# Kernel tuning notes

Hardware: AMD Instinct MI355X
Metric: run time of the kernel (lower is better)

The kernel has to match this reference:

```python
import jax, jax.numpy as jnp
import numpy as np
from jax.ops import segment_sum, segment_max

DIM = 32   # hidden dim (hardcoded in Net)
N = 10000  # nodes
E = 160000 # edges
B = 64     # graphs in batch


def setup_inputs():
    key = jax.random.key(0)
    ks = jax.random.split(key, 16)
    r = lambda k, s: jax.random.normal(k, s, dtype=jnp.float32) * 0.1
    z = lambda s: jnp.zeros(s, jnp.float32)
    return {
        "x": jax.random.normal(ks[0], (N, 1), jnp.float32),
        "edge_attr": jax.random.normal(ks[1], (E, 2), jnp.float32),
        "lin0_w": r(ks[2], (1, DIM)), "lin0_b": z((DIM,)),
        "nn_w1": r(ks[3], (2, 128)), "nn_b1": z((128,)),
        "nn_w2": r(ks[4], (128, DIM * DIM)), "nn_b2": z((DIM * DIM,)),
        "conv_root": r(ks[5], (DIM, DIM)), "conv_bias": z((DIM,)),
        "gru_w_ih": r(ks[6], (DIM, 3 * DIM)), "gru_w_hh": r(ks[7], (DIM, 3 * DIM)),
        "gru_b_ih": z((3 * DIM,)), "gru_b_hh": z((3 * DIM,)),
        "lstm_w_ih": r(ks[8], (2 * DIM, 4 * DIM)), "lstm_w_hh": r(ks[9], (DIM, 4 * DIM)),
        "lstm_b_ih": z((4 * DIM,)), "lstm_b_hh": z((4 * DIM,)),
        "lin1_w": r(ks[10], (2 * DIM, DIM)), "lin1_b": z((DIM,)),
        "lin2_w": r(ks[11], (DIM, 1)), "lin2_b": z((1,)),
        "edge_index": jax.random.randint(ks[12], (2, E), 0, N),
        "batch": jnp.sort(jax.random.randint(ks[13], (N,), 0, B)),
    }


def _forward(x, edge_attr, params, edge_index, batch):
    (lin0_w, lin0_b, nn_w1, nn_b1, nn_w2, nn_b2, conv_root, conv_bias,
     gru_w_ih, gru_w_hh, gru_b_ih, gru_b_hh,
     lstm_w_ih, lstm_w_hh, lstm_b_ih, lstm_b_hh,
     lin1_w, lin1_b, lin2_w, lin2_b) = params
    src, dst = edge_index[0], edge_index[1]
    deg = jnp.maximum(segment_sum(jnp.ones((E,), x.dtype), dst, num_segments=N), 1.0)[:, None]
    # edge-conditioned weight matrices (depend only on edge_attr -> compute once)
    ew = (jax.nn.relu(edge_attr @ nn_w1 + nn_b1) @ nn_w2 + nn_b2).reshape(E, DIM, DIM)

    out = jax.nn.relu(x @ lin0_w + lin0_b)  # (N, DIM)
    h = out                                  # GRU hidden state
    for _ in range(3):
        # NNConv: gather -> per-edge matmul -> scatter-mean, plus root weight + bias
        msg = jnp.einsum('ei,eio->eo', out[src], ew)          # (E, DIM)
        agg = segment_sum(msg, dst, num_segments=N) / deg      # (N, DIM)
        m = jax.nn.relu(agg + out @ conv_root + conv_bias)
        # single GRU step (seq_len = 1)
        gi = m @ gru_w_ih + gru_b_ih
        gh = h @ gru_w_hh + gru_b_hh
        i_r, i_z, i_n = jnp.split(gi, 3, axis=-1)
        h_r, h_z, h_n = jnp.split(gh, 3, axis=-1)
        rg = jax.nn.sigmoid(i_r + h_r)
        zg = jax.nn.sigmoid(i_z + h_z)
        ng = jnp.tanh(i_n + rg * h_n)
        h = (1.0 - zg) * ng + zg * h
        out = h

    # Set2Set pooling, 3 processing steps
    q_star = jnp.zeros((B, 2 * DIM), x.dtype)
    hh = jnp.zeros((B, DIM), x.dtype)
    cc = jnp.zeros((B, DIM), x.dtype)
    for _ in range(3):
        gates = q_star @ lstm_w_ih + lstm_b_ih + hh @ lstm_w_hh + lstm_b_hh
        ig, fg, gg, og = jnp.split(gates, 4, axis=-1)  # torch gate order i,f,g,o
        cc = jax.nn.sigmoid(fg) * cc + jax.nn.sigmoid(ig) * jnp.tanh(gg)
        hh = jax.nn.sigmoid(og) * jnp.tanh(cc)
        q = hh                                          # (B, DIM)
        e = jnp.sum(out * q[batch], axis=-1)            # (N,)
        a = jnp.exp(e - segment_max(e, batch, num_segments=B)[batch])
        a = a / segment_sum(a, batch, num_segments=B)[batch]
        rvec = segment_sum(a[:, None] * out, batch, num_segments=B)  # (B, DIM)
        q_star = jnp.concatenate([q, rvec], axis=-1)

    y = jax.nn.relu(q_star @ lin1_w + lin1_b)
    return (y @ lin2_w + lin2_b).reshape(-1)  # (B,)


def reference(x, edge_attr, lin0_w, lin0_b, nn_w1, nn_b1, nn_w2, nn_b2, conv_root, conv_bias, gru_w_ih, gru_w_hh, gru_b_ih, gru_b_hh, lstm_w_ih, lstm_w_hh, lstm_b_ih, lstm_b_hh, lin1_w, lin1_b, lin2_w, lin2_b, edge_index, batch):
    params = (lin0_w, lin0_b, nn_w1, nn_b1, nn_w2, nn_b2, conv_root, conv_bias,
              gru_w_ih, gru_w_hh, gru_b_ih, gru_b_hh,
              lstm_w_ih, lstm_w_hh, lstm_b_ih, lstm_b_hh,
              lin1_w, lin1_b, lin2_w, lin2_b)
    return _forward(x, edge_attr, params, edge_index, batch)
```

## Files before the change

kernel.cpp:

```cpp
#include <hip/hip_runtime.h>
#include <math.h>

#define NN 10000
#define NE 160000
#define NG 64
#define DIM 32
#define CAP 96
#define NBIN (CAP + 1)

typedef __attribute__((ext_vector_type(8))) short bf16x8;
typedef __attribute__((ext_vector_type(4))) float f32x4;
typedef __attribute__((ext_vector_type(2))) float f32x2;

__device__ __forceinline__ float sigmoidf_(float x) { return 1.f / (1.f + expf(-x)); }

__device__ __forceinline__ unsigned short f2bf(float x) {
    unsigned u = __float_as_uint(x);
    u += 0x7FFF + ((u >> 16) & 1);
    return (unsigned short)(u >> 16);
}
__device__ __forceinline__ float bf2f(unsigned short b) {
    return __uint_as_float(((unsigned)b) << 16);
}
__device__ __forceinline__ float rlanef(float v, int i) {
    return __uint_as_float((unsigned)__builtin_amdgcn_readlane((int)__float_as_uint(v), i));
}

__global__ void k_setup(const float* __restrict__ w2, unsigned short* __restrict__ w2f,
                        const float* __restrict__ x, const float* __restrict__ lw,
                        const float* __restrict__ lb, float* __restrict__ out,
                        const int* __restrict__ batch, int* __restrict__ gstart,
                        const int* __restrict__ ei, const float* __restrict__ ea,
                        int* __restrict__ cursor,
                        int* __restrict__ srt_src, float* __restrict__ srt_ea) {
    int b = blockIdx.x, t = threadIdx.x;
    if (b < 512) {
        int tid = b * 256 + t;
        int h = tid >> 10, rem = tid & 1023, i = rem >> 5, n = rem & 31;
        float v = w2[tid];
        unsigned short hi = f2bf(v);
        unsigned short lo = f2bf(v - bf2f(hi));
        int hp = 2 * (h & 63) + (h >> 6);
        int s = hp >> 5, hm = hp & 31, q = hm >> 3, j = hm & 7;
        int tile = n >> 4, nn = n & 15, lane = q * 16 + nn;
        int c = (i * 4 + s) * 2 + tile;
        w2f[(c * 2 + 0) * 512 + lane * 8 + j] = hi;
        w2f[(c * 2 + 1) * 512 + lane * 8 + j] = lo;
    } else if (b < 1762) {
        int idx = (b - 512) * 256 + t;
        int n = idx >> 5, d = idx & 31;
        out[idx] = fmaxf(x[n] * lw[d] + lb[d], 0.f);
    } else if (b == 1762) {
        if (t <= NG) {
            int g = t, lo = 0, hi = NN;
            while (lo < hi) { int mid = (lo + hi) >> 1; if (batch[mid] < g) lo = mid + 1; else hi = mid; }
            gstart[g] = lo;
        }
    } else {
        int e = (b - 1763) * 256 + t;
        if (e < NE) {
            int d = ei[NE + e];
            int p = atomicAdd(&cursor[d], 1);
            int pos = d * CAP + p;
            srt_src[pos] = ei[e];
            srt_ea[2 * pos]     = ea[2 * e];
            srt_ea[2 * pos + 1] = ea[2 * e + 1];
        }
    }
}

__global__ __launch_bounds__(1024) void k_perm(const int* __restrict__ cursor,
                                               int* __restrict__ perm) {
    __shared__ int hist[NBIN * 16];
    __shared__ int binsum[NBIN];
    __shared__ int base[NBIN];
    int t = threadIdx.x;
    for (int i = t; i < NBIN * 16; i += 1024) hist[i] = 0;
    __syncthreads();
    int sub = t & 15;
    for (int n = t; n < NN; n += 1024) {
        int d = cursor[n]; d = d > CAP ? CAP : d;
        atomicAdd(&hist[d * 16 + sub], 1);
    }
    __syncthreads();
    if (t < NBIN) {
        int s = 0;
        #pragma unroll
        for (int k = 0; k < 16; ++k) s += hist[t * 16 + k];
        binsum[t] = s;
    }
    __syncthreads();
    if (t == 0) {
        int acc = 0;
        for (int d = CAP; d >= 0; --d) { base[d] = acc; acc += binsum[d]; }
    }
    __syncthreads();
    if (t < NBIN) {
        int acc = base[t];
        #pragma unroll
        for (int k = 0; k < 16; ++k) {
            int c = hist[t * 16 + k];
            hist[t * 16 + k] = acc;
            acc += c;
        }
    }
    __syncthreads();
    for (int n = t; n < NN; n += 1024) {
        int d = cursor[n]; d = d > CAP ? CAP : d;
        int pos = atomicAdd(&hist[d * 16 + sub], 1);
        perm[pos] = n;
    }
}

#define NS 1040
#define PS 8320
__global__ __launch_bounds__(512, 4) void k_conv_gru(
    const int* __restrict__ perm,
    const int* __restrict__ cursor, const int* __restrict__ srt_src,
    const float* __restrict__ srt_ea,
    const float* __restrict__ w1, const float* __restrict__ b1,
    const unsigned short* __restrict__ w2f, const float* __restrict__ b2,
    const float* __restrict__ out_old,
    const float* __restrict__ root, const float* __restrict__ cbias,
    const float* __restrict__ wih, const float* __restrict__ whh,
    const float* __restrict__ bih, const float* __restrict__ bhh,
    float* __restrict__ out_new)
{
    __shared__ __align__(16) unsigned short RB[2 * PS];
    __shared__ float sSg[8][DIM];
    __shared__ int sNode[8];
    int t = threadIdx.x;
    int wave = t >> 6, lane = t & 63;
    int n0 = blockIdx.x * 8;
    int n = perm[n0 + wave];
    if (lane == 0) sNode[wave] = n;

    f32x2 acc2[32];
    #pragma unroll
    for (int i = 0; i < 32; ++i) acc2[i] = (f32x2){0.f, 0.f};
    float sacc = 0.f;

    float w1a0 = w1[lane],      w1c0 = w1[128 + lane],  bb0 = b1[lane];
    float w1a1 = w1[64 + lane], w1c1 = w1[192 + lane],  bb1 = b1[64 + lane];

    int deg = cursor[n];
    int rs = n * CAP;
    const float2* eap = (const float2*)srt_ea;

    int msrc = 0; float mex = 0.f, mey = 0.f;
    if (lane < deg) {
        msrc = srt_src[rs + lane];
        float2 a = eap[rs + lane];
        mex = a.x; mey = a.y;
    }

    int dmain = deg < 64 ? deg : 64;
    int i = 0;
    for (; i + 1 < dmain; i += 2) {
        int s0 = __builtin_amdgcn_readlane(msrc, i);
        int s1 = __builtin_amdgcn_readlane(msrc, i + 1);
        float a0x = rlanef(mex, i),     a0y = rlanef(mey, i);
        float a1x = rlanef(mex, i + 1), a1y = rlanef(mey, i + 1);
        const float* o0 = out_old + s0 * DIM;
        const float* o1 = out_old + s1 * DIM;
        f32x2 r0 = { fmaxf(a0x * w1a0 + a0y * w1c0 + bb0, 0.f),
                     fmaxf(a0x * w1a1 + a0y * w1c1 + bb1, 0.f) };
        f32x2 r1 = { fmaxf(a1x * w1a0 + a1y * w1c0 + bb0, 0.f),
                     fmaxf(a1x * w1a1 + a1y * w1c1 + bb1, 0.f) };
        #pragma unroll
        for (int q = 0; q < 32; ++q)
            acc2[q] += r0 * o0[q];
        #pragma unroll
        for (int q = 0; q < 32; ++q)
            acc2[q] += r1 * o1[q];
        const float* oc = (lane < 32) ? (o0 + lane) : (o1 + lane - 32);
        sacc += *oc;
    }
    if (i < dmain) {
        int s0 = __builtin_amdgcn_readlane(msrc, i);
        float a0x = rlanef(mex, i), a0y = rlanef(mey, i);
        const float* o0 = out_old + s0 * DIM;
        f32x2 r0 = { fmaxf(a0x * w1a0 + a0y * w1c0 + bb0, 0.f),
                     fmaxf(a0x * w1a1 + a0y * w1c1 + bb1, 0.f) };
        #pragma unroll
        for (int q = 0; q < 32; ++q)
            acc2[q] += r0 * o0[q];
        if (lane < 32) sacc += o0[lane];
    }
    for (int p = rs + 64; p < rs + deg; ++p) {
        int s0 = __builtin_amdgcn_readfirstlane(srt_src[p]);
        float2 a0 = eap[p];
        const float* o0 = out_old + s0 * DIM;
        f32x2 r0 = { fmaxf(a0.x * w1a0 + a0.y * w1c0 + bb0, 0.f),
                     fmaxf(a0.x * w1a1 + a0.y * w1c1 + bb1, 0.f) };
        #pragma unroll
        for (int q = 0; q < 32; ++q)
            acc2[q] += r0 * o0[q];
        if (lane < 32) sacc += o0[lane];
    }
    sacc += __shfl_xor(sacc, 32);
    if (lane < DIM) sSg[wave][lane] = sacc;

    int quad = lane >> 4;
    int mm = lane & 7;
    unsigned aoff = (unsigned)(mm * NS + wave * 128 + quad * 8);
    f32x4 acc0 = {0.f, 0.f, 0.f, 0.f};
    f32x4 acc1 = {0.f, 0.f, 0.f, 0.f};

    unsigned short* Hw = RB + wave * NS;
    unsigned short* Lw = RB + PS + wave * NS;

    #pragma unroll
    for (int pass = 0; pass < 4; ++pass) {
        if (pass) __syncthreads();
        #pragma unroll
        for (int li = 0; li < 8; ++li) {
            f32x2 v = acc2[pass * 8 + li];
            unsigned short h0 = f2bf(v.x);
            unsigned short l0 = f2bf(v.x - bf2f(h0));
            unsigned short h1 = f2bf(v.y);
            unsigned short l1 = f2bf(v.y - bf2f(h1));
            *(unsigned*)(Hw + li * 128 + 2 * lane) = (unsigned)h0 | ((unsigned)h1 << 16);
            *(unsigned*)(Lw + li * 128 + 2 * lane) = (unsigned)l0 | ((unsigned)l1 << 16);
        }
        __syncthreads();
        int ig = pass * 8 + wave;
        #pragma unroll
        for (int s = 0; s < 4; ++s) {
            bf16x8 ah = *(const bf16x8*)(RB + aoff + s * 32);
            bf16x8 al = *(const bf16x8*)(RB + PS + aoff + s * 32);
            const unsigned short* bp = w2f + (unsigned)((ig * 4 + s) * 2048 + lane * 8);
            bf16x8 bh0 = *(const bf16x8*)(bp);
            bf16x8 bl0 = *(const bf16x8*)(bp + 512);
            bf16x8 bh1 = *(const bf16x8*)(bp + 1024);
            bf16x8 bl1 = *(const bf16x8*)(bp + 1536);
            acc0 = __builtin_amdgcn_mfma_f32_16x16x32_bf16(ah, bh0, acc0, 0, 0, 0);
            acc0 = __builtin_amdgcn_mfma_f32_16x16x32_bf16(ah, bl0, acc0, 0, 0, 0);
            acc0 = __builtin_amdgcn_mfma_f32_16x16x32_bf16(al, bh0, acc0, 0, 0, 0);
            acc1 = __builtin_amdgcn_mfma_f32_16x16x32_bf16(ah, bh1, acc1, 0, 0, 0);
            acc1 = __builtin_amdgcn_mfma_f32_16x16x32_bf16(ah, bl1, acc1, 0, 0, 0);
            acc1 = __builtin_amdgcn_mfma_f32_16x16x32_bf16(al, bh1, acc1, 0, 0, 0);
        }
    }
    __syncthreads();

    float* part = (float*)RB;
    #pragma unroll
    for (int r = 0; r < 4; ++r) {
        part[((wave * 2 + 0) * 64 + lane) * 4 + r] = acc0[r];
        part[((wave * 2 + 1) * 64 + lane) * 4 + r] = acc1[r];
    }
    __syncthreads();

    if (t < 256) {
        int nb = t >> 5, d = t & 31;
        int nn_ = sNode[nb];
        int base = t & 32;
        int tile = d >> 4, col = d & 15;
        int lidx = (nb >> 2) * 16 + col, reg = nb & 3;
        float aggv = 0.f;
        #pragma unroll
        for (int wv = 0; wv < 8; ++wv)
            aggv += part[((wv * 2 + tile) * 64 + lidx) * 4 + reg];

        float bt = 0.f;
        #pragma unroll 8
        for (int i2 = 0; i2 < DIM; ++i2) bt += sSg[nb][i2] * b2[i2 * DIM + d];
        int cdeg = cursor[nn_];
        float degf = (float)(cdeg > 0 ? cdeg : 1);
        aggv = (aggv + bt) / degf;

        float x = out_old[nn_ * DIM + d];
        float rootsum = 0.f;
        #pragma unroll 8
        for (int k = 0; k < DIM; ++k)
            rootsum += __shfl(x, base + k) * root[k * DIM + d];
        float m = fmaxf(aggv + rootsum + cbias[d], 0.f);

        float gir = bih[d], giz = bih[DIM + d], gin = bih[2 * DIM + d];
        float ghr = bhh[d], ghz = bhh[DIM + d], ghn = bhh[2 * DIM + d];
        #pragma unroll 4
        for (int k = 0; k < DIM; ++k) {
            float mk = __shfl(m, base + k);
            float hk = __shfl(x, base + k);
            gir += mk * wih[k * 96 + d];
            giz += mk * wih[k * 96 + DIM + d];
            gin += mk * wih[k * 96 + 2 * DIM + d];
            ghr += hk * whh[k * 96 + d];
            ghz += hk * whh[k * 96 + DIM + d];
            ghn += hk * whh[k * 96 + 2 * DIM + d];
        }
        float rg = sigmoidf_(gir + ghr);
        float zg = sigmoidf_(giz + ghz);
        float ng = tanhf(gin + rg * ghn);
        out_new[nn_ * DIM + d] = (1.f - zg) * ng + zg * x;
    }
}

__global__ __launch_bounds__(256) void k_set2set(
    const float* __restrict__ out, const int* __restrict__ gstart,
    const float* __restrict__ wih, const float* __restrict__ whh,
    const float* __restrict__ bih, const float* __restrict__ bhh,
    const float* __restrict__ l1w, const float* __restrict__ l1b,
    const float* __restrict__ l2w, const float* __restrict__ l2b,
    float* __restrict__ ebuf, float* __restrict__ y)
{
    __shared__ float swih[64 * 128];
    __shared__ float swhh[32 * 128];
    __shared__ float sq[2 * DIM];
    __shared__ float shh[DIM], scc[DIM];
    __shared__ float sgates[4 * DIM];
    __shared__ float sacc[8][DIM];
    __shared__ float sredA[4], sredB[4];

    int g = blockIdx.x, t = threadIdx.x;
    {
        const float4* wv = (const float4*)wih;   float4* sv = (float4*)swih;
        for (int i = t; i < 2048; i += 256) sv[i] = wv[i];
        const float4* wv2 = (const float4*)whh;  float4* sv2 = (float4*)swhh;
        for (int i = t; i < 1024; i += 256) sv2[i] = wv2[i];
    }
    if (t < 2 * DIM) sq[t] = 0.f;
    if (t < DIM) { shh[t] = 0.f; scc[t] = 0.f; }
    int ns = gstart[g], ne = gstart[g + 1];
    __syncthreads();

    for (int step = 0; step < 3; ++step) {
        if (t < 128) {
            float acc = bih[t] + bhh[t];
            #pragma unroll 8
            for (int k = 0; k < 2 * DIM; ++k) acc += sq[k] * swih[k * 128 + t];
            #pragma unroll 8
            for (int k = 0; k < DIM; ++k)     acc += shh[k] * swhh[k * 128 + t];
            sgates[t] = acc;
        }
        __syncthreads();
        if (t < DIM) {
            float ig = sigmoidf_(sgates[t]);
            float fg = sigmoidf_(sgates[DIM + t]);
            float gg = tanhf(sgates[2 * DIM + t]);
            float og = sigmoidf_(sgates[3 * DIM + t]);
            float c_new = fg * scc[t] + ig * gg;
            float h_new = og * tanhf(c_new);
            scc[t] = c_new;
            shh[t] = h_new;
            sq[t] = h_new;
        }
        __syncthreads();

        float lmax = -3.0e38f;
        for (int n = ns + t; n < ne; n += 256) {
            const float4* orow = (const float4*)(out + n * DIM);
            float e = 0.f;
            #pragma unroll
            for (int q = 0; q < 8; ++q) {
                float4 o4 = orow[q];
                e += o4.x * shh[4 * q] + o4.y * shh[4 * q + 1]
                   + o4.z * shh[4 * q + 2] + o4.w * shh[4 * q + 3];
            }
            ebuf[n] = e;
            lmax = fmaxf(lmax, e);
        }
        #pragma unroll
        for (int s = 1; s < 64; s <<= 1) lmax = fmaxf(lmax, __shfl_xor(lmax, s));
        if ((t & 63) == 0) sredA[t >> 6] = lmax;
        __syncthreads();
        float M = fmaxf(fmaxf(sredA[0], sredA[1]), fmaxf(sredA[2], sredA[3]));

        float lsum = 0.f;
        for (int n = ns + t; n < ne; n += 256) {
            float v = expf(ebuf[n] - M);
            ebuf[n] = v;
            lsum += v;
        }
        #pragma unroll
        for (int s = 1; s < 64; s <<= 1) lsum += __shfl_xor(lsum, s);
        if ((t & 63) == 0) sredB[t >> 6] = lsum;
        __syncthreads();
        float S = sredB[0] + sredB[1] + sredB[2] + sredB[3];
        float inv = (S > 0.f) ? 1.f / S : 0.f;

        int stp = t >> 5, d = t & 31;
        float racc = 0.f;
        for (int n = ns + stp; n < ne; n += 8)
            racc += ebuf[n] * out[n * DIM + d];
        sacc[stp][d] = racc;
        __syncthreads();
        if (t < DIM) {
            float r = 0.f;
            #pragma unroll
            for (int s = 0; s < 8; ++s) r += sacc[s][t];
            sq[DIM + t] = r * inv;
        }
        __syncthreads();
    }

    if (t < DIM) {
        float h = l1b[t];
        #pragma unroll 8
        for (int k = 0; k < 2 * DIM; ++k) h += sq[k] * l1w[k * DIM + t];
        float v = fmaxf(h, 0.f) * l2w[t];
        #pragma unroll
        for (int s = 1; s < 32; s <<= 1) v += __shfl_xor(v, s);
        if (t == 0) y[g] = v + l2b[0];
    }
}

extern "C" void kernel_launch(void* const* d_in, const int* in_sizes, int n_in,
                              void* d_out, int out_size, void* d_ws, size_t ws_size,
                              hipStream_t stream) {
    const float* x         = (const float*)d_in[0];
    const float* edge_attr = (const float*)d_in[1];
    const float* lin0_w    = (const float*)d_in[2];
    const float* lin0_b    = (const float*)d_in[3];
    const float* nn_w1     = (const float*)d_in[4];
    const float* nn_b1     = (const float*)d_in[5];
    const float* nn_w2     = (const float*)d_in[6];
    const float* nn_b2     = (const float*)d_in[7];
    const float* conv_root = (const float*)d_in[8];
    const float* conv_bias = (const float*)d_in[9];
    const float* gru_w_ih  = (const float*)d_in[10];
    const float* gru_w_hh  = (const float*)d_in[11];
    const float* gru_b_ih  = (const float*)d_in[12];
    const float* gru_b_hh  = (const float*)d_in[13];
    const float* lstm_w_ih = (const float*)d_in[14];
    const float* lstm_w_hh = (const float*)d_in[15];
    const float* lstm_b_ih = (const float*)d_in[16];
    const float* lstm_b_hh = (const float*)d_in[17];
    const float* lin1_w    = (const float*)d_in[18];
    const float* lin1_b    = (const float*)d_in[19];
    const float* lin2_w    = (const float*)d_in[20];
    const float* lin2_b    = (const float*)d_in[21];
    const int*   edge_index= (const int*)d_in[22];
    const int*   batch     = (const int*)d_in[23];
    float* yout = (float*)d_out;

    char* p = (char*)d_ws;
    auto alloc = [&](size_t bytes) { char* r = p; p += (bytes + 255) & ~(size_t)255; return r; };

    int*   cursor = (int*)  alloc(NN * sizeof(int));
    size_t zero_bytes = (size_t)(p - (char*)d_ws);
    int*   gstart    = (int*)  alloc((NG + 1) * sizeof(int));
    int*   srt_src   = (int*)  alloc((size_t)NN * CAP * sizeof(int));
    float* srt_ea    = (float*)alloc((size_t)NN * CAP * 2 * sizeof(float));
    float* outA      = (float*)alloc(NN * DIM * sizeof(float));
    float* outB      = (float*)alloc(NN * DIM * sizeof(float));
    int*   perm      = (int*)  alloc(NN * sizeof(int));
    unsigned short* w2f = (unsigned short*)alloc(262144 * sizeof(unsigned short));
    float* ebuf      = (float*)alloc(NN * sizeof(float));
    (void)ws_size; (void)n_in; (void)in_sizes; (void)out_size;

    hipMemsetAsync(d_ws, 0, zero_bytes, stream);

    k_setup<<<2388, 256, 0, stream>>>(nn_w2, w2f, x, lin0_w, lin0_b, outA, batch, gstart,
                                      edge_index, edge_attr, cursor, srt_src, srt_ea);
    k_perm<<<1, 1024, 0, stream>>>(cursor, perm);

    const float* cur = outA;
    float* nxt = outB;
    for (int it = 0; it < 3; ++it) {
        k_conv_gru<<<1250, 512, 0, stream>>>(perm, cursor, srt_src, srt_ea,
                                             nn_w1, nn_b1, w2f, nn_b2,
                                             cur,
                                             conv_root, conv_bias,
                                             gru_w_ih, gru_w_hh, gru_b_ih, gru_b_hh,
                                             nxt);
        const float* tmp = nxt; nxt = (float*)cur; cur = tmp;
    }
    const float* outF = cur;

    k_set2set<<<NG, 256, 0, stream>>>(outF, gstart,
                                      lstm_w_ih, lstm_w_hh, lstm_b_ih, lstm_b_hh,
                                      lin1_w, lin1_b, lin2_w, lin2_b, ebuf, yout);
}
```

Baseline: 319.0 us.

## Split each node's hidden units across two waves in conv_gru blocks

Each node's 128-wide edge-network hidden dimension is now split across two waves, so blocks grow to 1024 threads (16 waves) and each thread keeps 32 accumulators instead of 64 packed pairs. The w2f weight layout is reordered to match the new hidden-unit ownership, and each wave runs only half of the MFMA k-slices. The partial-sum reduction now covers 16 waves. The goal is lower register pressure and more waves in flight to hide gather latency. The cost is that both waves gather the same neighbour rows, duplicating loads, and larger blocks add barrier overhead.

```diff
diff --git a/kernel.cpp b/kernel.cpp
--- a/kernel.cpp
+++ b/kernel.cpp
@@ -10,7 +10,6 @@
 
 typedef __attribute__((ext_vector_type(8))) short bf16x8;
 typedef __attribute__((ext_vector_type(4))) float f32x4;
-typedef __attribute__((ext_vector_type(2))) float f32x2;
 
 __device__ __forceinline__ float sigmoidf_(float x) { return 1.f / (1.f + expf(-x)); }
 
@@ -40,8 +39,7 @@
         float v = w2[tid];
         unsigned short hi = f2bf(v);
         unsigned short lo = f2bf(v - bf2f(hi));
-        int hp = 2 * (h & 63) + (h >> 6);
-        int s = hp >> 5, hm = hp & 31, q = hm >> 3, j = hm & 7;
+        int s = h >> 5, hm = h & 31, q = hm >> 3, j = hm & 7;
         int tile = n >> 4, nn = n & 15, lane = q * 16 + nn;
         int c = (i * 4 + s) * 2 + tile;
         w2f[(c * 2 + 0) * 512 + lane * 8 + j] = hi;
@@ -114,7 +112,7 @@
 
 #define NS 1040
 #define PS 8320
-__global__ __launch_bounds__(512, 4) void k_conv_gru(
+__global__ __launch_bounds__(1024, 8) void k_conv_gru(
     const int* __restrict__ perm,
     const int* __restrict__ cursor, const int* __restrict__ srt_src,
     const float* __restrict__ srt_ea,
@@ -130,18 +128,18 @@
     __shared__ float sSg[8][DIM];
     __shared__ int sNode[8];
     int t = threadIdx.x;
-    int wave = t >> 6, lane = t & 63;
-    int n0 = blockIdx.x * 8;
-    int n = perm[n0 + wave];
-    if (lane == 0) sNode[wave] = n;
-
-    f32x2 acc2[32];
+    int w = t >> 6, lane = t & 63;
+    int nslot = w & 7, hhalf = w >> 3;
+    int n = perm[blockIdx.x * 8 + nslot];
+    if (hhalf == 0 && lane == 0) sNode[nslot] = n;
+    int hb = hhalf * 64;
+
+    float acc[32];
     #pragma unroll
-    for (int i = 0; i < 32; ++i) acc2[i] = (f32x2){0.f, 0.f};
+    for (int q = 0; q < 32; ++q) acc[q] = 0.f;
     float sacc = 0.f;
 
-    float w1a0 = w1[lane],      w1c0 = w1[128 + lane],  bb0 = b1[lane];
-    float w1a1 = w1[64 + lane], w1c1 = w1[192 + lane],  bb1 = b1[64 + lane];
+    float w1a = w1[hb + lane], w1c = w1[128 + hb + lane], bb = b1[hb + lane];
 
     int deg = cursor[n];
     int rs = n * CAP;
@@ -163,70 +161,64 @@
         float a1x = rlanef(mex, i + 1), a1y = rlanef(mey, i + 1);
         const float* o0 = out_old + s0 * DIM;
         const float* o1 = out_old + s1 * DIM;
-        f32x2 r0 = { fmaxf(a0x * w1a0 + a0y * w1c0 + bb0, 0.f),
-                     fmaxf(a0x * w1a1 + a0y * w1c1 + bb1, 0.f) };
-        f32x2 r1 = { fmaxf(a1x * w1a0 + a1y * w1c0 + bb0, 0.f),
-                     fmaxf(a1x * w1a1 + a1y * w1c1 + bb1, 0.f) };
-        #pragma unroll
-        for (int q = 0; q < 32; ++q)
-            acc2[q] += r0 * o0[q];
-        #pragma unroll
-        for (int q = 0; q < 32; ++q)
-            acc2[q] += r1 * o1[q];
-        const float* oc = (lane < 32) ? (o0 + lane) : (o1 + lane - 32);
-        sacc += *oc;
+        float r0 = fmaxf(a0x * w1a + a0y * w1c + bb, 0.f);
+        float r1 = fmaxf(a1x * w1a + a1y * w1c + bb, 0.f);
+        #pragma unroll
+        for (int q = 0; q < 32; ++q) acc[q] += r0 * o0[q];
+        #pragma unroll
+        for (int q = 0; q < 32; ++q) acc[q] += r1 * o1[q];
+        if (hhalf == 0) {
+            const float* oc = (lane < 32) ? (o0 + lane) : (o1 + lane - 32);
+            sacc += *oc;
+        }
     }
     if (i < dmain) {
         int s0 = __builtin_amdgcn_readlane(msrc, i);
         float a0x = rlanef(mex, i), a0y = rlanef(mey, i);
         const float* o0 = out_old + s0 * DIM;
-        f32x2 r0 = { fmaxf(a0x * w1a0 + a0y * w1c0 + bb0, 0.f),
-                     fmaxf(a0x * w1a1 + a0y * w1c1 + bb1, 0.f) };
-        #pragma unroll
-        for (int q = 0; q < 32; ++q)
-            acc2[q] += r0 * o0[q];
-        if (lane < 32) sacc += o0[lane];
+        float r0 = fmaxf(a0x * w1a + a0y * w1c + bb, 0.f);
+        #pragma unroll
+        for (int q = 0; q < 32; ++q) acc[q] += r0 * o0[q];
+        if (hhalf == 0 && lane < 32) sacc += o0[lane];
     }
     for (int p = rs + 64; p < rs + deg; ++p) {
         int s0 = __builtin_amdgcn_readfirstlane(srt_src[p]);
         float2 a0 = eap[p];
         const float* o0 = out_old + s0 * DIM;
-        f32x2 r0 = { fmaxf(a0.x * w1a0 + a0.y * w1c0 + bb0, 0.f),
-                     fmaxf(a0.x * w1a1 + a0.y * w1c1 + bb1, 0.f) };
-        #pragma unroll
-        for (int q = 0; q < 32; ++q)
-            acc2[q] += r0 * o0[q];
-        if (lane < 32) sacc += o0[lane];
-    }
-    sacc += __shfl_xor(sacc, 32);
-    if (lane < DIM) sSg[wave][lane] = sacc;
+        float r0 = fmaxf(a0.x * w1a + a0.y * w1c + bb, 0.f);
+        #pragma unroll
+        for (int q = 0; q < 32; ++q) acc[q] += r0 * o0[q];
+        if (hhalf == 0 && lane < 32) sacc += o0[lane];
+    }
+    if (hhalf == 0) {
+        sacc += __shfl_xor(sacc, 32);
+        if (lane < DIM) sSg[nslot][lane] = sacc;
+    }
 
     int quad = lane >> 4;
-    int mm = lane & 7;
-    unsigned aoff = (unsigned)(mm * NS + wave * 128 + quad * 8);
+    unsigned aoff = (unsigned)((lane & 7) * NS + nslot * 128 + quad * 8);
     f32x4 acc0 = {0.f, 0.f, 0.f, 0.f};
     f32x4 acc1 = {0.f, 0.f, 0.f, 0.f};
 
-    unsigned short* Hw = RB + wave * NS;
-    unsigned short* Lw = RB + PS + wave * NS;
+    unsigned short* Hw = RB + nslot * NS + hb;
+    unsigned short* Lw = RB + PS + nslot * NS + hb;
 
     #pragma unroll
     for (int pass = 0; pass < 4; ++pass) {
         if (pass) __syncthreads();
         #pragma unroll
         for (int li = 0; li < 8; ++li) {
-            f32x2 v = acc2[pass * 8 + li];
-            unsigned short h0 = f2bf(v.x);
-            unsigned short l0 = f2bf(v.x - bf2f(h0));
-            unsigned short h1 = f2bf(v.y);
-            unsigned short l1 = f2bf(v.y - bf2f(h1));
-            *(unsigned*)(Hw + li * 128 + 2 * lane) = (unsigned)h0 | ((unsigned)h1 << 16);
-            *(unsigned*)(Lw + li * 128 + 2 * lane) = (unsigned)l0 | ((unsigned)l1 << 16);
-        }
-        __syncthreads();
-        int ig = pass * 8 + wave;
-        #pragma unroll
-        for (int s = 0; s < 4; ++s) {
+            float v = acc[pass * 8 + li];
+            unsigned short h0 = f2bf(v);
+            unsigned short l0 = f2bf(v - bf2f(h0));
+            Hw[li * 128 + lane] = h0;
+            Lw[li * 128 + lane] = l0;
+        }
+        __syncthreads();
+        int ig = pass * 8 + nslot;
+        #pragma unroll
+        for (int si = 0; si < 2; ++si) {
+            int s = hhalf * 2 + si;
             bf16x8 ah = *(const bf16x8*)(RB + aoff + s * 32);
             bf16x8 al = *(const bf16x8*)(RB + PS + aoff + s * 32);
             const unsigned short* bp = w2f + (unsigned)((ig * 4 + s) * 2048 + lane * 8);
@@ -247,8 +239,8 @@
     float* part = (float*)RB;
     #pragma unroll
     for (int r = 0; r < 4; ++r) {
-        part[((wave * 2 + 0) * 64 + lane) * 4 + r] = acc0[r];
-        part[((wave * 2 + 1) * 64 + lane) * 4 + r] = acc1[r];
+        part[((w * 2 + 0) * 64 + lane) * 4 + r] = acc0[r];
+        part[((w * 2 + 1) * 64 + lane) * 4 + r] = acc1[r];
     }
     __syncthreads();
 
@@ -260,7 +252,7 @@
         int lidx = (nb >> 2) * 16 + col, reg = nb & 3;
         float aggv = 0.f;
         #pragma unroll
-        for (int wv = 0; wv < 8; ++wv)
+        for (int wv = 0; wv < 16; ++wv)
             aggv += part[((wv * 2 + tile) * 64 + lidx) * 4 + reg];
 
         float bt = 0.f;
@@ -459,12 +451,12 @@
     const float* cur = outA;
     float* nxt = outB;
     for (int it = 0; it < 3; ++it) {
-        k_conv_gru<<<1250, 512, 0, stream>>>(perm, cursor, srt_src, srt_ea,
-                                             nn_w1, nn_b1, w2f, nn_b2,
-                                             cur,
-                                             conv_root, conv_bias,
-                                             gru_w_ih, gru_w_hh, gru_b_ih, gru_b_hh,
-                                             nxt);
+        k_conv_gru<<<1250, 1024, 0, stream>>>(perm, cursor, srt_src, srt_ea,
+                                              nn_w1, nn_b1, w2f, nn_b2,
+                                              cur,
+                                              conv_root, conv_bias,
+                                              gru_w_ih, gru_w_hh, gru_b_ih, gru_b_hh,
+                                              nxt);
         const float* tmp = nxt; nxt = (float*)cur; cur = tmp;
     }
     const float* outF = cur;
```

Result: slower. 330.0 us (+3.4%).

## Process 16 nodes per block so MFMA tiles use full 16-row A fragments

Applied to the files above, without the earlier changes.

The conv-GRU kernel now launches 1024-thread blocks that each handle 16 nodes instead of 8. The bf16 hi/lo MFMA stage uses all 16 rows of the A tile instead of replicating 8 nodes, and its k-slices are split across two wave groups. This halves the w2f weight fetches per node and the wasted MFMA rows. LDS is also re-padded (LIS/ANS strides) to reduce bank conflicts. The cost is roughly double the shared memory per block and a 16-way partial reduction, and 1024-thread blocks with launch bounds of 4 may cut occupancy and raise register pressure.

```diff
diff --git a/kernel.cpp b/kernel.cpp
--- a/kernel.cpp
+++ b/kernel.cpp
@@ -112,9 +112,10 @@
     }
 }
 
-#define NS 1040
-#define PS 8320
-__global__ __launch_bounds__(512, 4) void k_conv_gru(
+#define LIS 136
+#define ANS 1096
+#define PS2 (16 * ANS)
+__global__ __launch_bounds__(1024, 4) void k_conv_gru(
     const int* __restrict__ perm,
     const int* __restrict__ cursor, const int* __restrict__ srt_src,
     const float* __restrict__ srt_ea,
@@ -126,14 +127,13 @@
     const float* __restrict__ bih, const float* __restrict__ bhh,
     float* __restrict__ out_new)
 {
-    __shared__ __align__(16) unsigned short RB[2 * PS];
-    __shared__ float sSg[8][DIM];
-    __shared__ int sNode[8];
+    __shared__ __align__(16) unsigned short RB[2 * PS2];
+    __shared__ float sSg[16][DIM];
+    __shared__ int sNode[16];
     int t = threadIdx.x;
-    int wave = t >> 6, lane = t & 63;
-    int n0 = blockIdx.x * 8;
-    int n = perm[n0 + wave];
-    if (lane == 0) sNode[wave] = n;
+    int w = t >> 6, lane = t & 63;
+    int n = perm[blockIdx.x * 16 + w];
+    if (lane == 0) sNode[w] = n;
 
     f32x2 acc2[32];
     #pragma unroll
@@ -199,16 +199,15 @@
         if (lane < 32) sacc += o0[lane];
     }
     sacc += __shfl_xor(sacc, 32);
-    if (lane < DIM) sSg[wave][lane] = sacc;
+    if (lane < DIM) sSg[w][lane] = sacc;
 
     int quad = lane >> 4;
-    int mm = lane & 7;
-    unsigned aoff = (unsigned)(mm * NS + wave * 128 + quad * 8);
+    unsigned aoff = (unsigned)((lane & 15) * ANS + (w & 7) * LIS + quad * 8);
     f32x4 acc0 = {0.f, 0.f, 0.f, 0.f};
     f32x4 acc1 = {0.f, 0.f, 0.f, 0.f};
 
-    unsigned short* Hw = RB + wave * NS;
-    unsigned short* Lw = RB + PS + wave * NS;
+    unsigned short* Hw = RB + (unsigned)(w * ANS);
+    unsigned short* Lw = Hw + PS2;
 
     #pragma unroll
     for (int pass = 0; pass < 4; ++pass) {
@@ -220,15 +219,17 @@
             unsigned short l0 = f2bf(v.x - bf2f(h0));
             unsigned short h1 = f2bf(v.y);
             unsigned short l1 = f2bf(v.y - bf2f(h1));
-            *(unsigned*)(Hw + li * 128 + 2 * lane) = (unsigned)h0 | ((unsigned)h1 << 16);
-            *(unsigned*)(Lw + li * 128 + 2 * lane) = (unsigned)l0 | ((unsigned)l1 << 16);
-        }
-        __syncthreads();
-        int ig = pass * 8 + wave;
-        #pragma unroll
-        for (int s = 0; s < 4; ++s) {
+            *(unsigned*)(Hw + li * LIS + 2 * lane) = (unsigned)h0 | ((unsigned)h1 << 16);
+            *(unsigned*)(Lw + li * LIS + 2 * lane) = (unsigned)l0 | ((unsigned)l1 << 16);
+        }
+        __syncthreads();
+        int ig = pass * 8 + (w & 7);
+        int sb = (w >> 3) * 2;
+        #pragma unroll
+        for (int si = 0; si < 2; ++si) {
+            int s = sb + si;
             bf16x8 ah = *(const bf16x8*)(RB + aoff + s * 32);
-            bf16x8 al = *(const bf16x8*)(RB + PS + aoff + s * 32);
+            bf16x8 al = *(const bf16x8*)(RB + PS2 + aoff + s * 32);
             const unsigned short* bp = w2f + (unsigned)((ig * 4 + s) * 2048 + lane * 8);
             bf16x8 bh0 = *(const bf16x8*)(bp);
             bf16x8 bl0 = *(const bf16x8*)(bp + 512);
@@ -247,12 +248,12 @@
     float* part = (float*)RB;
     #pragma unroll
     for (int r = 0; r < 4; ++r) {
-        part[((wave * 2 + 0) * 64 + lane) * 4 + r] = acc0[r];
-        part[((wave * 2 + 1) * 64 + lane) * 4 + r] = acc1[r];
-    }
-    __syncthreads();
-
-    if (t < 256) {
+        part[((w * 2 + 0) * 64 + lane) * 4 + r] = acc0[r];
+        part[((w * 2 + 1) * 64 + lane) * 4 + r] = acc1[r];
+    }
+    __syncthreads();
+
+    if (t < 512) {
         int nb = t >> 5, d = t & 31;
         int nn_ = sNode[nb];
         int base = t & 32;
@@ -260,7 +261,7 @@
         int lidx = (nb >> 2) * 16 + col, reg = nb & 3;
         float aggv = 0.f;
         #pragma unroll
-        for (int wv = 0; wv < 8; ++wv)
+        for (int wv = 0; wv < 16; ++wv)
             aggv += part[((wv * 2 + tile) * 64 + lidx) * 4 + reg];
 
         float bt = 0.f;
@@ -459,7 +460,7 @@
     const float* cur = outA;
     float* nxt = outB;
     for (int it = 0; it < 3; ++it) {
-        k_conv_gru<<<1250, 512, 0, stream>>>(perm, cursor, srt_src, srt_ea,
+        k_conv_gru<<<625, 1024, 0, stream>>>(perm, cursor, srt_src, srt_ea,
                                              nn_w1, nn_b1, w2f, nn_b2,
                                              cur,
                                              conv_root, conv_bias,
```

After: 344.0 us. 1.08x slower.

## Stage gathered neighbor features in LDS via coalesced float4 loads

Applied to the files above, without the earlier changes.

Replaces the per-edge scalar global loads of neighbor feature rows with a cooperative gather. Each wave loads 32 source rows at once as float4 (8 rows per step, indices distributed by ds_bpermute) into an LDS staging area, then accumulates from LDS. The goal is to turn many serialized broadcast global loads into coalesced vector loads plus fast LDS reads. In exchange it reuses the RB shared buffer as staging, which needs an added __syncthreads before later passes overwrite it, and the row-sum reduction now reads back from LDS.

```diff
diff --git a/kernel.cpp b/kernel.cpp
--- a/kernel.cpp
+++ b/kernel.cpp
@@ -154,38 +154,40 @@
         mex = a.x; mey = a.y;
     }
 
+    float* stage = (float*)RB + wave * 1024;
     int dmain = deg < 64 ? deg : 64;
-    int i = 0;
-    for (; i + 1 < dmain; i += 2) {
-        int s0 = __builtin_amdgcn_readlane(msrc, i);
-        int s1 = __builtin_amdgcn_readlane(msrc, i + 1);
-        float a0x = rlanef(mex, i),     a0y = rlanef(mey, i);
-        float a1x = rlanef(mex, i + 1), a1y = rlanef(mey, i + 1);
-        const float* o0 = out_old + s0 * DIM;
-        const float* o1 = out_old + s1 * DIM;
-        f32x2 r0 = { fmaxf(a0x * w1a0 + a0y * w1c0 + bb0, 0.f),
-                     fmaxf(a0x * w1a1 + a0y * w1c1 + bb1, 0.f) };
-        f32x2 r1 = { fmaxf(a1x * w1a0 + a1y * w1c0 + bb0, 0.f),
-                     fmaxf(a1x * w1a1 + a1y * w1c1 + bb1, 0.f) };
-        #pragma unroll
-        for (int q = 0; q < 32; ++q)
-            acc2[q] += r0 * o0[q];
-        #pragma unroll
-        for (int q = 0; q < 32; ++q)
-            acc2[q] += r1 * o1[q];
-        const float* oc = (lane < 32) ? (o0 + lane) : (o1 + lane - 32);
-        sacc += *oc;
-    }
-    if (i < dmain) {
-        int s0 = __builtin_amdgcn_readlane(msrc, i);
-        float a0x = rlanef(mex, i), a0y = rlanef(mey, i);
-        const float* o0 = out_old + s0 * DIM;
-        f32x2 r0 = { fmaxf(a0x * w1a0 + a0y * w1c0 + bb0, 0.f),
-                     fmaxf(a0x * w1a1 + a0y * w1c1 + bb1, 0.f) };
-        #pragma unroll
-        for (int q = 0; q < 32; ++q)
-            acc2[q] += r0 * o0[q];
-        if (lane < 32) sacc += o0[lane];
+
+    for (int c = 0; c < dmain; c += 32) {
+        int cn = dmain - c; cn = cn < 32 ? cn : 32;
+        int nk = (cn + 7) >> 3;
+        for (int k = 0; k < nk; ++k) {
+            int eidx = c + k * 8 + (lane >> 3);
+            int ecl = eidx < deg ? eidx : deg - 1;
+            int rid = __builtin_amdgcn_ds_bpermute(ecl << 2, msrc);
+            float4 v = *(const float4*)(out_old + rid * DIM + (lane & 7) * 4);
+            *(float4*)(stage + (k * 8 + (lane >> 3)) * DIM + (lane & 7) * 4) = v;
+        }
+        for (int e = 0; e < cn; ++e) {
+            int eg = c + e;
+            float ax = rlanef(mex, eg);
+            float ay = rlanef(mey, eg);
+            f32x2 r0 = { fmaxf(ax * w1a0 + ay * w1c0 + bb0, 0.f),
+                         fmaxf(ax * w1a1 + ay * w1c1 + bb1, 0.f) };
+            const float* sx = stage + e * DIM;
+            #pragma unroll
+            for (int q = 0; q < 32; ++q)
+                acc2[q] += r0 * sx[q];
+        }
+        {
+            int half16 = (lane >> 5) * 16;
+            int dd = lane & 31;
+            #pragma unroll
+            for (int jj = 0; jj < 16; ++jj) {
+                int row = half16 + jj;
+                float v = stage[row * DIM + dd];
+                if (c + row < dmain) sacc += v;
+            }
+        }
     }
     for (int p = rs + 64; p < rs + deg; ++p) {
         int s0 = __builtin_amdgcn_readfirstlane(srt_src[p]);
@@ -200,6 +202,7 @@
     }
     sacc += __shfl_xor(sacc, 32);
     if (lane < DIM) sSg[wave][lane] = sacc;
+    __syncthreads();
 
     int quad = lane >> 4;
     int mm = lane & 7;
```

Result: slower. 343.6 us (+7.7%).
